# Performance work log

Measured on AMD Instinct MI355X. Metric: run time of the kernel, lower is better.

## Reference

```python
import jax, jax.numpy as jnp
import numpy as np

M, IN, OUT = 8192, 4096, 4096
BITWIDTH = 7


def psto_shift_int32(x, shift):
    """Pseudo-stochastic right-shift of int32 x by `shift` bits -> int8.
    Faithful to PstoShiftInt32: floor-divide, derive a pseudo random number
    from the low half of the remainder, compare against the high half."""
    pow_s = jnp.left_shift(jnp.int32(1), shift)
    rt = jnp.floor_divide(x, pow_s)
    prob = jnp.abs(x - rt * pow_s)
    half_pow = jnp.left_shift(jnp.int32(1), shift // 2)
    qp = jnp.floor_divide(prob, half_pow)
    prn = prob - qp * half_pow
    prn = jnp.where(shift % 2 == 1, prn * 2, prn)
    dec = jnp.where(qp <= prn, jnp.int32(0), jnp.int32(1)) * jnp.sign(x)
    return jnp.clip(rt + dec, -127, 127).astype(jnp.int8)


def range_bitwidth(x):
    # RangeEstimate: ceil(log2(max|x|)), 0 if all-zero (torch also goes via float)
    m = jnp.max(jnp.abs(x)).astype(jnp.float32)
    return jnp.where(m == 0, jnp.int32(0), jnp.ceil(jnp.log2(m)).astype(jnp.int32))


def act_calc(acc, exp_in):
    """Shift int32 accumulator back to int8 and track the block exponent."""
    bw = range_bitwidth(acc)
    shift = bw - BITWIDTH
    # shift>1 -> shift by `shift`; shift==1 -> shift by 2; else -> plain int8 cast
    eff = jnp.where(shift > 1, shift, jnp.where(shift == 1, jnp.int32(2), jnp.int32(0)))
    rounded = psto_shift_int32(acc, jnp.maximum(eff, 0))
    out = jnp.where(eff > 0, rounded, acc.astype(jnp.int8))  # int8 cast wraps, as in torch
    exp_out = (exp_in + eff).astype(jnp.int8)
    return out, exp_out


def setup_inputs() -> dict:
    key = jax.random.key(0)
    k1, k2 = jax.random.split(key)
    # int8-valued tensors kept in int32 containers for the matmul accumulate
    act_in = jax.random.randint(k1, (M, IN), -127, 128, dtype=jnp.int32)
    weight = jax.random.randint(k2, (OUT, IN), -127, 128, dtype=jnp.int32)
    return {"act_in": act_in, "exp_in": -6, "weight": weight, "weight_exp": -9}


def reference(act_in, exp_in, weight, weight_exp):
    # the roundoff4 padding in the original is a no-op)
    acc = jnp.matmul(act_in, weight.T)  # [M, OUT] int32
    act_out, exp_out = act_calc(acc, jnp.int32(exp_in) + jnp.int32(weight_exp))
    return act_out, exp_out
```

## Files before the change

kernel.cpp:

```cpp
#include <hip/hip_runtime.h>
#include <stdint.h>
#include <math.h>

#define M_DIM 8192
#define N_DIM 4096
#define K_DIM 4096
#define BITWIDTH 7

#define BM 256
#define BN 128
#define BK 128
#define NT (K_DIM / BK)

using i32x4  = __attribute__((ext_vector_type(4)))  int;
using i32x16 = __attribute__((ext_vector_type(16))) int;

#define FENCE asm volatile("" ::: "memory")

__global__ __launch_bounds__(256) void pack_both_kernel(
        const int* __restrict__ act, const int* __restrict__ wt,
        uint32_t* __restrict__ a8p, uint32_t* __restrict__ w8,
        int* __restrict__ maxabs) {
    if (blockIdx.x == 0 && threadIdx.x == 0) *maxabs = 0;

    if (blockIdx.x < 8192) {
        const int tid = blockIdx.x * 256 + threadIdx.x;
        const int L  = tid & 63;
        const int kb = (tid >> 6) & 127;
        const int mb = tid >> 13;
        const size_t src = (size_t)(mb * 32 + (L & 31)) * K_DIM
                         + kb * 32 + (L >> 5) * 16;
        const int4* s = (const int4*)(act + src);
        uint32_t w[4];
#pragma unroll
        for (int q = 0; q < 4; ++q) {
            int4 v = s[q];
            w[q] = (uint32_t)(v.x & 0xFF) | ((uint32_t)(v.y & 0xFF) << 8)
                 | ((uint32_t)(v.z & 0xFF) << 16) | ((uint32_t)(v.w & 0xFF) << 24);
        }
        ((uint4*)a8p)[tid] = make_uint4(w[0], w[1], w[2], w[3]);
    } else {
        const int i = (blockIdx.x - 8192) * 256 + threadIdx.x;
        int4 a = ((const int4*)wt)[2 * i];
        int4 b = ((const int4*)wt)[2 * i + 1];
        uint32_t p0 = (uint32_t)(a.x & 0xFF) | ((uint32_t)(a.y & 0xFF) << 8)
                    | ((uint32_t)(a.z & 0xFF) << 16) | ((uint32_t)(a.w & 0xFF) << 24);
        uint32_t p1 = (uint32_t)(b.x & 0xFF) | ((uint32_t)(b.y & 0xFF) << 8)
                    | ((uint32_t)(b.z & 0xFF) << 16) | ((uint32_t)(b.w & 0xFF) << 24);
        ((uint2*)w8)[i] = make_uint2(p0, p1);
    }
}

__device__ __forceinline__ void gload_lds16(const int8_t* g, int8_t* lds) {
    __builtin_amdgcn_global_load_lds(
        (__attribute__((address_space(1))) void*)g,
        (__attribute__((address_space(3))) void*)lds,
        16, 0, 0);
}

__device__ __forceinline__ void load_af(i32x4 (&d)[4], const int8_t* aBase,
                                        int tkk) {
#pragma unroll
    for (int i = 0; i < 4; ++i)
        d[i] = *(const i32x4*)(aBase + (size_t)((i * 128 + tkk) << 10));
}

__device__ __forceinline__ void kkstep(const i32x4 (&a)[4], const int8_t* bbuf,
                                       const int (&bo)[2], i32x16 (&acc)[4][2]) {
    i32x4 b0 = *(const i32x4*)(bbuf + bo[0]);
    i32x4 b1 = *(const i32x4*)(bbuf + bo[1]);
#pragma unroll
    for (int i = 0; i < 4; ++i) {
        acc[i][0] = __builtin_amdgcn_mfma_i32_32x32x32_i8(a[i], b0, acc[i][0], 0, 0, 0);
        acc[i][1] = __builtin_amdgcn_mfma_i32_32x32x32_i8(a[i], b1, acc[i][1], 0, 0, 0);
    }
}

__global__ __launch_bounds__(256, 2) void gemm_i8(
        const int8_t* __restrict__ A8p, const int8_t* __restrict__ B8,
        int* __restrict__ C, int* __restrict__ maxabs) {
    __shared__ __align__(16) int8_t Bs[2][BN * BK];
    __shared__ int wmaxs[4];
    int8_t* BsF = &Bs[0][0];

    const int tid  = threadIdx.x;
    const int wave = tid >> 6;
    const int lane = tid & 63;
    const int fr   = lane & 31;
    const int hl   = lane >> 5;

    const int row0 = blockIdx.y * BM;
    const int col0 = blockIdx.x * BN;

    const int wm = (wave >> 1) * 128;
    const int wn = (wave & 1) * 64;

    i32x16 acc[4][2];
#pragma unroll
    for (int i = 0; i < 4; ++i)
#pragma unroll
        for (int j = 0; j < 2; ++j)
            acc[i][j] = (i32x16)(0);

    const int srowoff = lane >> 3;
    const int schk    = ((lane & 7) ^ srowoff) << 4;
    const int8_t* bg  = B8 + (size_t)(col0 + wave * 8 + srowoff) * K_DIM + schk;
    const int ldsoB   = wave * 1024;

    const int mbase = (row0 + wm) >> 5;
    const int8_t* aBase = A8p + (size_t)mbase * 128 * 1024 + (size_t)lane * 16;

    const int swz = fr & 7;
    int boff[4][2];
#pragma unroll
    for (int kk = 0; kk < 4; ++kk) {
        const int co = (((kk * 2 + hl) ^ swz) << 4);
#pragma unroll
        for (int j = 0; j < 2; ++j)
            boff[kk][j] = (wn + j * 32 + fr) * BK + co;
    }

    i32x4 afE[4], afO[4];

#pragma unroll
    for (int g = 0; g < 4; ++g)
        gload_lds16(bg + (size_t)(32 * g) * K_DIM, BsF + ldsoB + g * 4096);
    FENCE;
    load_af(afE, aBase, 0);
    asm volatile("s_waitcnt vmcnt(4)" ::: "memory");
    __builtin_amdgcn_s_barrier();

    for (int t = 0; t < NT - 1; ++t) {
        const int8_t* bbuf = BsF + ((t & 1) << 14);
        int8_t* bstg = BsF + (((t + 1) & 1) << 14) + ldsoB;
        const int kg = (t + 1) * BK;
#pragma unroll
        for (int g = 0; g < 4; ++g)
            gload_lds16(bg + kg + (size_t)(32 * g) * K_DIM, bstg + g * 4096);
        FENCE;
        load_af(afO, aBase, t * 4 + 1); FENCE;
        kkstep(afE, bbuf, boff[0], acc);
        load_af(afE, aBase, t * 4 + 2); FENCE;
        kkstep(afO, bbuf, boff[1], acc);
        load_af(afO, aBase, t * 4 + 3); FENCE;
        kkstep(afE, bbuf, boff[2], acc);
        load_af(afE, aBase, t * 4 + 4); FENCE;
        kkstep(afO, bbuf, boff[3], acc);
        asm volatile("s_waitcnt vmcnt(4)" ::: "memory");
        __builtin_amdgcn_s_barrier();
    }

    {
        const int tl = NT - 1;
        const int8_t* bbuf = BsF + ((tl & 1) << 14);
        load_af(afO, aBase, tl * 4 + 1);
        kkstep(afE, bbuf, boff[0], acc);
        load_af(afE, aBase, tl * 4 + 2);
        kkstep(afO, bbuf, boff[1], acc);
        load_af(afO, aBase, tl * 4 + 3);
        kkstep(afE, bbuf, boff[2], acc);
        kkstep(afO, bbuf, boff[3], acc);
    }

    int mymax = 0;
    const int ccol = fr;
    const int rbase = hl << 2;
#pragma unroll
    for (int i = 0; i < 4; ++i) {
#pragma unroll
        for (int j = 0; j < 2; ++j) {
            int* p = C + (size_t)(row0 + wm + i * 32) * N_DIM
                       + (col0 + wn + j * 32 + ccol);
#pragma unroll
            for (int r = 0; r < 16; ++r) {
                int row = (r & 3) + 8 * (r >> 2) + rbase;
                int v = acc[i][j][r];
                p[(size_t)row * N_DIM] = v;
                int a = v < 0 ? -v : v;
                mymax = a > mymax ? a : mymax;
            }
        }
    }

#pragma unroll
    for (int off = 32; off > 0; off >>= 1) {
        int o = __shfl_down(mymax, off, 64);
        mymax = o > mymax ? o : mymax;
    }
    if (lane == 0) wmaxs[wave] = mymax;
    __syncthreads();
    if (tid == 0) {
        int bmx = wmaxs[0];
        for (int w = 1; w < 4; ++w) bmx = wmaxs[w] > bmx ? wmaxs[w] : bmx;
        atomicMax(maxabs, bmx);
    }
}

__device__ __forceinline__ int psto(int x, int eff) {
    if (eff > 0) {
        int rt   = x >> eff;
        int prob = x & ((1 << eff) - 1);
        int h    = eff >> 1;
        int qp   = prob >> h;
        int prn  = (prob & ((1 << h) - 1)) << (eff & 1);
        int sgn  = (x > 0) - (x < 0);
        int r    = rt + ((qp <= prn) ? 0 : sgn);
        r = r < -127 ? -127 : r;
        r = r > 127 ? 127 : r;
        return r;
    }
    return (int)(int8_t)x;
}

__global__ __launch_bounds__(256) void finalize_kernel(int* __restrict__ C,
        const int* __restrict__ maxabs,
        const int* __restrict__ exp_in,
        const int* __restrict__ wexp) {
    const int m = *maxabs;
    int bw = 0;
    if (m != 0) bw = (int)ceilf(log2f((float)m));
    const int shift = bw - BITWIDTH;
    const int eff = (shift > 1) ? shift : ((shift == 1) ? 2 : 0);

    const size_t idx = ((size_t)blockIdx.x * blockDim.x + threadIdx.x) * 8;
    int4 v0 = *(const int4*)(C + idx);
    int4 v1 = *(const int4*)(C + idx + 4);
    int4 o0, o1;
    o0.x = psto(v0.x, eff); o0.y = psto(v0.y, eff);
    o0.z = psto(v0.z, eff); o0.w = psto(v0.w, eff);
    o1.x = psto(v1.x, eff); o1.y = psto(v1.y, eff);
    o1.z = psto(v1.z, eff); o1.w = psto(v1.w, eff);
    *(int4*)(C + idx) = o0;
    *(int4*)(C + idx + 4) = o1;

    if (idx == 0) {
        C[(size_t)M_DIM * N_DIM] = (int)(int8_t)(exp_in[0] + wexp[0] + eff);
    }
}

extern "C" void kernel_launch(void* const* d_in, const int* in_sizes, int n_in,
                              void* d_out, int out_size, void* d_ws, size_t ws_size,
                              hipStream_t stream) {
    const int* act    = (const int*)d_in[0];
    const int* exp_in = (const int*)d_in[1];
    const int* wt     = (const int*)d_in[2];
    const int* wexp   = (const int*)d_in[3];

    int8_t* a8p    = (int8_t*)d_ws;
    int8_t* w8     = a8p + (size_t)M_DIM * K_DIM;
    int*    maxabs = (int*)(w8 + (size_t)N_DIM * K_DIM);

    pack_both_kernel<<<16384, 256, 0, stream>>>(
        act, wt, (uint32_t*)a8p, (uint32_t*)w8, maxabs);

    int* C = (int*)d_out;
    dim3 grid(N_DIM / BN, M_DIM / BM);
    gemm_i8<<<grid, 256, 0, stream>>>(a8p, w8, C, maxabs);

    finalize_kernel<<<((size_t)M_DIM * N_DIM / 8) / 256, 256, 0, stream>>>(
        C, maxabs, exp_in, wexp);
}
```

Measured before the change: 440.1 us.

## Reshape wave tiling to 64x128 per wave with double-buffered B fragments

Changes the per-wave tile from 128x64 (4 A fragments x 2 B fragments) to 64x128 (2 A fragments x 4 B fragments), so every wave reads the whole B tile from LDS and streams half as many A fragments from global memory. B fragments are now preloaded into registers in an even/odd double-buffer ahead of each MFMA step, and the vmcnt waits are adjusted to the smaller number of in-flight A loads. This trades fewer global A loads per wave for more LDS reads of B and more fragment registers.

```diff
diff --git a/kernel.cpp b/kernel.cpp
--- a/kernel.cpp
+++ b/kernel.cpp
@@ -58,22 +58,28 @@
         16, 0, 0);
 }
 
-__device__ __forceinline__ void load_af(i32x4 (&d)[4], const int8_t* aBase,
+__device__ __forceinline__ void load_af(i32x4 (&d)[2], const int8_t* aBase,
                                         int tkk) {
 #pragma unroll
-    for (int i = 0; i < 4; ++i)
+    for (int i = 0; i < 2; ++i)
         d[i] = *(const i32x4*)(aBase + (size_t)((i * 128 + tkk) << 10));
 }
 
-__device__ __forceinline__ void kkstep(const i32x4 (&a)[4], const int8_t* bbuf,
-                                       const int (&bo)[2], i32x16 (&acc)[4][2]) {
-    i32x4 b0 = *(const i32x4*)(bbuf + bo[0]);
-    i32x4 b1 = *(const i32x4*)(bbuf + bo[1]);
-#pragma unroll
-    for (int i = 0; i < 4; ++i) {
-        acc[i][0] = __builtin_amdgcn_mfma_i32_32x32x32_i8(a[i], b0, acc[i][0], 0, 0, 0);
-        acc[i][1] = __builtin_amdgcn_mfma_i32_32x32x32_i8(a[i], b1, acc[i][1], 0, 0, 0);
-    }
+__device__ __forceinline__ void load_bf(i32x4 (&d)[4], const int8_t* bbuf,
+                                        const int (&ro)[4], int co) {
+#pragma unroll
+    for (int j = 0; j < 4; ++j)
+        d[j] = *(const i32x4*)(bbuf + ro[j] + co);
+}
+
+__device__ __forceinline__ void kkstep(const i32x4 (&a)[2], const i32x4 (&b)[4],
+                                       i32x16 (&acc)[2][4]) {
+#pragma unroll
+    for (int i = 0; i < 2; ++i)
+#pragma unroll
+        for (int j = 0; j < 4; ++j)
+            acc[i][j] = __builtin_amdgcn_mfma_i32_32x32x32_i8(
+                a[i], b[j], acc[i][j], 0, 0, 0);
 }
 
 __global__ __launch_bounds__(256, 2) void gemm_i8(
@@ -92,14 +98,13 @@
     const int row0 = blockIdx.y * BM;
     const int col0 = blockIdx.x * BN;
 
-    const int wm = (wave >> 1) * 128;
-    const int wn = (wave & 1) * 64;
-
-    i32x16 acc[4][2];
-#pragma unroll
-    for (int i = 0; i < 4; ++i)
-#pragma unroll
-        for (int j = 0; j < 2; ++j)
+    const int wm = wave * 64;
+
+    i32x16 acc[2][4];
+#pragma unroll
+    for (int i = 0; i < 2; ++i)
+#pragma unroll
+        for (int j = 0; j < 4; ++j)
             acc[i][j] = (i32x16)(0);
 
     const int srowoff = lane >> 3;
@@ -107,70 +112,79 @@
     const int8_t* bg  = B8 + (size_t)(col0 + wave * 8 + srowoff) * K_DIM + schk;
     const int ldsoB   = wave * 1024;
 
-    const int mbase = (row0 + wm) >> 5;
-    const int8_t* aBase = A8p + (size_t)mbase * 128 * 1024 + (size_t)lane * 16;
+    const int mbase = (row0 >> 5) + wave * 2;
+    const int8_t* aBase = A8p + ((size_t)mbase << 17) + (size_t)lane * 16;
 
     const int swz = fr & 7;
-    int boff[4][2];
-#pragma unroll
-    for (int kk = 0; kk < 4; ++kk) {
-        const int co = (((kk * 2 + hl) ^ swz) << 4);
-#pragma unroll
-        for (int j = 0; j < 2; ++j)
-            boff[kk][j] = (wn + j * 32 + fr) * BK + co;
-    }
-
-    i32x4 afE[4], afO[4];
+    int rowOff[4];
+#pragma unroll
+    for (int j = 0; j < 4; ++j)
+        rowOff[j] = (j * 32 + fr) * BK;
+    int co[4];
+#pragma unroll
+    for (int kk = 0; kk < 4; ++kk)
+        co[kk] = ((kk * 2 + hl) ^ swz) << 4;
+
+    i32x4 afE[2], afO[2], bfE[4], bfO[4];
 
 #pragma unroll
     for (int g = 0; g < 4; ++g)
         gload_lds16(bg + (size_t)(32 * g) * K_DIM, BsF + ldsoB + g * 4096);
     FENCE;
     load_af(afE, aBase, 0);
-    asm volatile("s_waitcnt vmcnt(4)" ::: "memory");
+    asm volatile("s_waitcnt vmcnt(2)" ::: "memory");
     __builtin_amdgcn_s_barrier();
 
     for (int t = 0; t < NT - 1; ++t) {
         const int8_t* bbuf = BsF + ((t & 1) << 14);
         int8_t* bstg = BsF + (((t + 1) & 1) << 14) + ldsoB;
         const int kg = (t + 1) * BK;
+
+        load_bf(bfE, bbuf, rowOff, co[0]); FENCE;
+        load_af(afO, aBase, t * 4 + 1);    FENCE;
 #pragma unroll
         for (int g = 0; g < 4; ++g)
             gload_lds16(bg + kg + (size_t)(32 * g) * K_DIM, bstg + g * 4096);
         FENCE;
-        load_af(afO, aBase, t * 4 + 1); FENCE;
-        kkstep(afE, bbuf, boff[0], acc);
-        load_af(afE, aBase, t * 4 + 2); FENCE;
-        kkstep(afO, bbuf, boff[1], acc);
-        load_af(afO, aBase, t * 4 + 3); FENCE;
-        kkstep(afE, bbuf, boff[2], acc);
-        load_af(afE, aBase, t * 4 + 4); FENCE;
-        kkstep(afO, bbuf, boff[3], acc);
-        asm volatile("s_waitcnt vmcnt(4)" ::: "memory");
+        load_bf(bfO, bbuf, rowOff, co[1]); FENCE;
+        kkstep(afE, bfE, acc);
+        load_af(afE, aBase, t * 4 + 2);
+        load_bf(bfE, bbuf, rowOff, co[2]); FENCE;
+        kkstep(afO, bfO, acc);
+        load_af(afO, aBase, t * 4 + 3);
+        load_bf(bfO, bbuf, rowOff, co[3]); FENCE;
+        kkstep(afE, bfE, acc);
+        load_af(afE, aBase, t * 4 + 4);    FENCE;
+        kkstep(afO, bfO, acc);
+        asm volatile("s_waitcnt vmcnt(2)" ::: "memory");
         __builtin_amdgcn_s_barrier();
     }
 
     {
         const int tl = NT - 1;
         const int8_t* bbuf = BsF + ((tl & 1) << 14);
+        load_bf(bfE, bbuf, rowOff, co[0]);
         load_af(afO, aBase, tl * 4 + 1);
-        kkstep(afE, bbuf, boff[0], acc);
+        load_bf(bfO, bbuf, rowOff, co[1]); FENCE;
+        kkstep(afE, bfE, acc);
         load_af(afE, aBase, tl * 4 + 2);
-        kkstep(afO, bbuf, boff[1], acc);
+        load_bf(bfE, bbuf, rowOff, co[2]); FENCE;
+        kkstep(afO, bfO, acc);
         load_af(afO, aBase, tl * 4 + 3);
-        kkstep(afE, bbuf, boff[2], acc);
-        kkstep(afO, bbuf, boff[3], acc);
+        load_bf(bfO, bbuf, rowOff, co[3]); FENCE;
+        kkstep(afE, bfE, acc);
+        kkstep(afO, bfO, acc);
     }
 
     int mymax = 0;
     const int ccol = fr;
     const int rbase = hl << 2;
 #pragma unroll
-    for (int i = 0; i < 4; ++i) {
-#pragma unroll
-        for (int j = 0; j < 2; ++j) {
+    for (int i = 0; i < 2; ++i) {
+#pragma unroll
+        for (int j = 0; j < 4; ++j) {
             int* p = C + (size_t)(row0 + wm + i * 32) * N_DIM
-                       + (col0 + wn + j * 32 + ccol);
+                       + (col0 + j * 32 + ccol);
 #pragma unroll
             for (int r = 0; r < 16; ++r) {
                 int row = (r & 3) + 8 * (r >> 2) + rbase;
```

Measured after the change: 434.2 us. About the same (-1.3%).
